# Kernel tuning notes

Measured on AMD Instinct MI355X. Metric: run time of the kernel, lower is better.

## Reference

```python
import jax, jax.numpy as jnp
import numpy as np


def _icosa_group():
    """60 rotation matrices of the icosahedral rotation group (vertex anchors)."""
    phi = (1.0 + 5.0 ** 0.5) / 2.0

    def rot(axis, ang):
        a = np.asarray(axis, dtype=np.float64)
        a = a / np.linalg.norm(a)
        K = np.array([[0.0, -a[2], a[1]], [a[2], 0.0, -a[0]], [-a[1], a[0], 0.0]])
        return np.eye(3) + np.sin(ang) * K + (1.0 - np.cos(ang)) * (K @ K)

    # two distinct 5-fold vertex axes generate the full group of order 60
    gens = [rot([0.0, 1.0, phi], 2.0 * np.pi / 5.0),
            rot([0.0, -1.0, phi], 2.0 * np.pi / 5.0)]
    mats = {tuple(np.round(np.eye(3), 6).ravel()): np.eye(3)}
    frontier = [np.eye(3)]
    while frontier:
        new = []
        for m in frontier:
            for g in gens:
                p = g @ m
                k = tuple(np.round(p, 6).ravel())
                if k not in mats:
                    mats[k] = p
                    new.append(p)
        frontier = new
    Rs = np.stack([mats[k] for k in sorted(mats.keys())]).astype(np.float32)
    assert Rs.shape[0] == 60
    return Rs


def _normalize(x, axis=-1, eps=1e-12):
    n = jnp.linalg.norm(x, axis=axis, keepdims=True)
    return x / jnp.maximum(n, eps)


def setup_inputs() -> dict:
    key = jax.random.key(0)
    ks = jax.random.split(key, 6)
    bs, P, N = 2, 1024, 16
    d_in, d_out, K = 64, 32, 7
    neighbor_index = jax.random.randint(ks[0], (bs, P, N), 0, P, dtype=jnp.int32)
    vertices = jax.random.normal(ks[1], (bs, P, 3), dtype=jnp.float32)
    feature_map = jax.random.normal(ks[2], (bs, d_in, P, 3), dtype=jnp.float32)
    W = jax.random.normal(ks[3], (d_out, d_in, K, 3), dtype=jnp.float32) * (2.0 / (d_in * K * 3 + d_out * K * 3)) ** 0.5
    W_center = jax.random.normal(ks[4], (d_out, d_in), dtype=jnp.float32) * (2.0 / (d_in + d_out)) ** 0.5
    directions = jax.random.normal(ks[5], (d_out, K, 3), dtype=jnp.float32) * (2.0 / (d_out * 3 + K * 3)) ** 0.5
    Rs = jnp.asarray(_icosa_group())
    return {"neighbor_index": neighbor_index, "vertices": vertices,
            "feature_map": feature_map, "W": W, "W_center": W_center,
            "directions": directions, "Rs": Rs}


def reference(neighbor_index, vertices, feature_map, W, W_center, directions, Rs):
    bs, P, N = neighbor_index.shape
    d_out, d_in, K, _ = W.shape
    n_bin = 5
    interval = Rs.shape[0] // n_bin

    # neighbor direction unit vectors [b,p,n,3]
    nbrs = jax.vmap(lambda v_b, i_b: v_b[i_b])(vertices, neighbor_index)
    ndn = _normalize(nbrs - vertices[:, :, None, :])
    kd = _normalize(directions)  # [d,k,3]

    # ---- stage 1: rotation search (fully detached in the torch original) ----
    ndn_s = jax.lax.stop_gradient(ndn)
    kd_s = jax.lax.stop_gradient(kd)
    W_s = jax.lax.stop_gradient(W)
    fm_s = jax.lax.stop_gradient(feature_map)
    Rs_s = jax.lax.stop_gradient(Rs)

    r_vals, r_idxs = [], []
    for i in range(n_bin):
        Rsi = Rs_s[i * interval:(i + 1) * interval]  # [r,3,3]
        kd_ro = jnp.einsum('dkj,rij->dkir', kd_s, Rsi)          # [d,k,3,r]
        theta = jnp.einsum('dkjr,bpnj->bdkpnr', kd_ro, ndn_s)   # [b,d,k,p,n,r]
        W_ro = jnp.einsum('dckj,rij->dckir', W_s, Rsi)          # [d,c,k,3,r]
        fo = jnp.einsum('dckir,bcpi->bdkpr', W_ro, fm_s)        # [b,d,k,p,r]
        gathered = jax.vmap(lambda f_b, i_b: f_b[:, :, i_b, :])(fo, neighbor_index)  # [b,d,k,p,n,r]
        ka = gathered * theta
        ka = jnp.max(ka, axis=4)   # max over neighbors -> [b,d,k,p,r]
        ka = jnp.sum(ka, axis=2)   # sum over kernel pts -> [b,d,p,r]
        r_vals.append(jnp.max(ka, axis=-1))
        r_idxs.append(jnp.argmax(ka, axis=-1) + i * interval)
    r_vals = jnp.stack(r_vals, axis=-1)  # [b,d,p,5]
    r_idxs = jnp.stack(r_idxs, axis=-1)  # [b,d,p,5]
    best_bin = jnp.argmax(r_vals, axis=-1)  # [b,d,p]
    r_index = jnp.take_along_axis(r_idxs, best_bin[..., None], axis=-1)[..., 0]  # [b,d,p]
    match_R = Rs[r_index]  # [b,d,p,3,3]

    # ---- stage 2: apply best rotation (differentiable) ----
    kd_ro2 = jnp.einsum('dkj,bdpij->bdkpi', kd, match_R)               # [b,d,k,p,3]
    theta2 = jax.nn.relu(jnp.einsum('bdkpj,bpnj->bdkpn', kd_ro2, ndn))  # [b,d,k,p,n]
    fo2 = jnp.einsum('dckj,bdpij,bcpi->bdkp', W, match_R, feature_map)  # [b,d,k,p]
    gathered2 = jax.vmap(lambda f_b, i_b: f_b[:, :, i_b])(fo2, neighbor_index)  # [b,d,k,p,n]
    ka2 = gathered2 * theta2
    kaw2 = jnp.max(ka2, axis=4)  # [b,d,k,p]
    out = jnp.einsum('bdkp,bdkpi->bdpi', kaw2, kd_ro2)
    center = jnp.einsum('dc,bcpi->bdpi', W_center, feature_map)
    return out + center
```

## Files before the change

### kernel.cpp

```cpp
#include <hip/hip_runtime.h>
#include <math.h>

#define BS   2
#define PP   1024
#define NN   16
#define CIN  64
#define DOUT 32
#define KK   7
#define NR   60
#define NT2  30

#define OFF_NDN  0
#define OFF_KROT 98304
#define OFF_M    138624
#define OFF_PVAL 4332928
#define OFF_PIDX 6299008
#define OFF_FO2  6790528
#define OFF_RIDX 7314816
#define OFF_CEN  7380352

#define NEG_INF (-3.402823466e38f)

typedef float v2f __attribute__((ext_vector_type(2)));
typedef float v4f __attribute__((ext_vector_type(4)));

__device__ __forceinline__ float sload(const float* __restrict__ p, int idx) {
    return __int_as_float(__builtin_amdgcn_readfirstlane(__float_as_int(p[idx])));
}

__device__ __forceinline__ v2f pk_mul_sv(v2f s, v2f v) {
    v2f d; asm("v_pk_mul_f32 %0, %1, %2" : "=v"(d) : "s"(s), "v"(v)); return d;
}
__device__ __forceinline__ v2f pk_fma_svv(v2f s, v2f v, v2f c) {
    v2f d; asm("v_pk_fma_f32 %0, %1, %2, %3" : "=v"(d) : "s"(s), "v"(v), "v"(c)); return d;
}
__device__ __forceinline__ v2f pk_mul_vv(v2f a, v2f b) {
    v2f d; asm("v_pk_mul_f32 %0, %1, %2" : "=v"(d) : "v"(a), "v"(b)); return d;
}

__device__ __forceinline__ float quad_max(float x) {
    float y = __int_as_float(__builtin_amdgcn_mov_dpp(
        __float_as_int(x), 0xB1, 0xF, 0xF, true));
    x = fmaxf(x, y);
    float z = __int_as_float(__builtin_amdgcn_mov_dpp(
        __float_as_int(x), 0x4E, 0xF, 0xF, true));
    return fmaxf(x, z);
}

__global__ __launch_bounds__(256) void k_pre(const int* __restrict__ nbr,
                                             const float* __restrict__ vert,
                                             const float* __restrict__ dirs,
                                             const float* __restrict__ Rs,
                                             float* __restrict__ ws) {
    int tid = blockIdx.x * 256 + threadIdx.x;
    if (tid < BS * PP * NN) {
        int p = (tid >> 4) & (PP - 1);
        int b = tid >> 14;
        int q = nbr[tid];
        const float* vp = vert + ((b << 10) + p) * 3;
        const float* vq = vert + ((b << 10) + q) * 3;
        float dx = vq[0] - vp[0], dy = vq[1] - vp[1], dz = vq[2] - vp[2];
        float nrm = sqrtf(dx * dx + dy * dy + dz * dz);
        float den = fmaxf(nrm, 1e-12f);
        dx /= den; dy /= den; dz /= den;
        float* o = ws + OFF_NDN + tid * 3;
        o[0] = dx; o[1] = dy; o[2] = dz;
    }
    int t2 = tid - BS * PP * NN;
    if (t2 >= 0 && t2 < DOUT * NR * KK) {
        int k = t2 % KK;
        int r = (t2 / KK) % NR;
        int d = t2 / (KK * NR);
        const float* dk = dirs + (d * KK + k) * 3;
        float x = dk[0], y = dk[1], z = dk[2];
        float nrm = sqrtf(x * x + y * y + z * z);
        float den = fmaxf(nrm, 1e-12f);
        x /= den; y /= den; z /= den;
        const float* R = Rs + r * 9;
        float* o = ws + OFF_KROT + t2 * 3;
        o[0] = R[0] * x + R[1] * y + R[2] * z;
        o[1] = R[3] * x + R[4] * y + R[5] * z;
        o[2] = R[6] * x + R[7] * y + R[8] * z;
    }
}

__global__ __launch_bounds__(256, 2) void k_buildM(const float* __restrict__ fm,
                                                   const float* __restrict__ W,
                                                   const float* __restrict__ Wc,
                                                   float* __restrict__ Mout,
                                                   float* __restrict__ cen) {
    int d = blockIdx.y, b = blockIdx.z;
    int p = blockIdx.x * 256 + threadIdx.x;

    float M[64];
#pragma unroll
    for (int t = 0; t < 64; t++) M[t] = 0.f;
    float c0 = 0.f, c1 = 0.f, c2 = 0.f;

    const float* fbase = fm + (size_t)(b * CIN * PP + p) * 3;
    const float* wbase = W + (size_t)d * CIN * KK * 3;
    const float* wrow = Wc + d * CIN;
    for (int c = 0; c < CIN; c++) {
        const float* f = fbase + c * PP * 3;
        float f0 = f[0], f1 = f[1], f2 = f[2];
        const float* wl = wbase + c * 21;
#pragma unroll
        for (int k = 0; k < KK; k++) {
#pragma unroll
            for (int j = 0; j < 3; j++) {
                float w = sload(wl, k * 3 + j);
                M[k * 9 + 0 + j] += w * f0;
                M[k * 9 + 3 + j] += w * f1;
                M[k * 9 + 6 + j] += w * f2;
            }
        }
        float wcv = sload(wrow, c);
        c0 += wcv * f0; c1 += wcv * f1; c2 += wcv * f2;
    }
    int gid = ((b * DOUT + d) << 10) + p;
    float4* o = (float4*)(Mout + (size_t)gid * 64);
#pragma unroll
    for (int t = 0; t < 15; t++)
        o[t] = make_float4(M[4 * t], M[4 * t + 1], M[4 * t + 2], M[4 * t + 3]);
    o[15] = make_float4(M[60], M[61], M[62], 0.f);
    float* cp = cen + (size_t)gid * 3;
    cp[0] = c0; cp[1] = c1; cp[2] = c2;
}

__device__ __forceinline__ int fo_base(int p) {
    return (p << 2) ^ ((p >> 1) & 7);
}

__global__ __launch_bounds__(1024)
void k_score(const int* __restrict__ nbr,
             const float* __restrict__ Rs,
             const float* __restrict__ Mptr,
             const float* __restrict__ ndn,
             const float* __restrict__ krot,
             float* __restrict__ pval,
             unsigned char* __restrict__ pidx8) {
    __shared__ v4f fo4s[PP * 4];
    const int tile = blockIdx.x, d = blockIdx.y, b = blockIdx.z;
    const int bd = b * DOUT + d;
    const int rbase = tile * 2;
    const int tq = threadIdx.x >> 2;
    const int ns = threadIdx.x & 3;

    {
        const int p = threadIdx.x;
        float Rc0[9], Rc1[9];
#pragma unroll
        for (int j = 0; j < 9; j++) {
            Rc0[j] = sload(Rs, (rbase + 0) * 9 + j);
            Rc1[j] = sload(Rs, (rbase + 1) * 9 + j);
        }
        float fo0[KK], fo1[KK];
#pragma unroll
        for (int k = 0; k < KK; k++) { fo0[k] = 0.f; fo1[k] = 0.f; }

        const float4* m4 = (const float4*)(Mptr + (size_t)((bd << 10) + p) * 64);
#pragma unroll
        for (int t = 0; t < 16; t++) {
            float4 v = m4[t];
            float e[4] = {v.x, v.y, v.z, v.w};
#pragma unroll
            for (int ee = 0; ee < 4; ee++) {
                const int g = 4 * t + ee;
                if (g < 63) {
                    const int k = g / 9, r9 = g % 9;
                    fo0[k] += Rc0[r9] * e[ee];
                    fo1[k] += Rc1[r9] * e[ee];
                }
            }
            if ((t & 3) == 3)
                __builtin_amdgcn_sched_barrier(0);
        }
        const int fb = fo_base(p);
        v4f s0; s0.x = fo0[0]; s0.y = fo1[0]; s0.z = fo0[1]; s0.w = fo1[1];
        v4f s1; s1.x = fo0[2]; s1.y = fo1[2]; s1.z = fo0[3]; s1.w = fo1[3];
        v4f s2; s2.x = fo0[4]; s2.y = fo1[4]; s2.z = fo0[5]; s2.w = fo1[5];
        v4f s3; s3.x = fo0[6]; s3.y = fo1[6]; s3.z = 0.f;    s3.w = 0.f;
        fo4s[fb]     = s0;
        fo4s[fb ^ 1] = s1;
        fo4s[fb ^ 2] = s2;
        fo4s[fb ^ 3] = s3;
    }
    __syncthreads();

    v2f vkp[KK][3];
    {
        const int kb0 = (d * NR + rbase + 0) * 21;
        const int kb1 = (d * NR + rbase + 1) * 21;
#pragma unroll
        for (int k = 0; k < KK; k++)
#pragma unroll
            for (int c = 0; c < 3; c++) {
                v2f t; t.x = sload(krot, kb0 + k * 3 + c);
                       t.y = sload(krot, kb1 + k * 3 + c);
                vkp[k][c] = t;
            }
    }
    const v2f* fo2s = (const v2f*)fo4s;

#pragma unroll
    for (int pp = 0; pp < 4; pp++) {
        const int p2 = (pp << 8) + tq;

        int4 nv = *(const int4*)(nbr + (((size_t)((b << 10) + p2)) << 4) + (ns << 2));
        float u[12];
        {
            const float4* u4 = (const float4*)(ndn + ((size_t)((b << 10) + p2) * 16 + (ns << 2)) * 3);
            float4 a = u4[0], bb = u4[1], cc = u4[2];
            u[0] = a.x;  u[1] = a.y;  u[2] = a.z;  u[3] = a.w;
            u[4] = bb.x; u[5] = bb.y; u[6] = bb.z; u[7] = bb.w;
            u[8] = cc.x; u[9] = cc.y; u[10] = cc.z; u[11] = cc.w;
        }

        float mk0[KK], mk1[KK];
#pragma unroll
        for (int k = 0; k < KK; k++) { mk0[k] = NEG_INF; mk1[k] = NEG_INF; }

        int c0 = fo_base(nv.x);
        v4f A = fo4s[c0];
        v4f B = fo4s[c0 ^ 1];
        v4f C = fo4s[c0 ^ 2];
        v2f D = fo2s[(c0 ^ 3) << 1];

#pragma unroll
        for (int n = 0; n < 4; n++) {
            v4f An, Bn, Cn; v2f Dn;
            if (n < 3) {
                int qn = (n == 0) ? nv.y : (n == 1) ? nv.z : nv.w;
                int cn = fo_base(qn);
                An = fo4s[cn];
                Bn = fo4s[cn ^ 1];
                Cn = fo4s[cn ^ 2];
                Dn = fo2s[(cn ^ 3) << 1];
            }
            float u0 = u[n * 3], u1 = u[n * 3 + 1], u2 = u[n * 3 + 2];
            v2f u00; u00.x = u0; u00.y = u0;
            v2f u11; u11.x = u1; u11.y = u1;
            v2f u22; u22.x = u2; u22.y = u2;
#pragma unroll
            for (int k = 0; k < KK; k++) {
                v2f g;
                if (k == 0)      g = __builtin_shufflevector(A, A, 0, 1);
                else if (k == 1) g = __builtin_shufflevector(A, A, 2, 3);
                else if (k == 2) g = __builtin_shufflevector(B, B, 0, 1);
                else if (k == 3) g = __builtin_shufflevector(B, B, 2, 3);
                else if (k == 4) g = __builtin_shufflevector(C, C, 0, 1);
                else if (k == 5) g = __builtin_shufflevector(C, C, 2, 3);
                else             g = D;
                v2f t = pk_mul_sv(vkp[k][0], u00);
                t = pk_fma_svv(vkp[k][1], u11, t);
                t = pk_fma_svv(vkp[k][2], u22, t);
                v2f pr = pk_mul_vv(g, t);
                mk0[k] = fmaxf(mk0[k], pr.x);
                mk1[k] = fmaxf(mk1[k], pr.y);
            }
            if (n < 3) { A = An; B = Bn; C = Cn; D = Dn; }
            __builtin_amdgcn_sched_barrier(0);
        }
#pragma unroll
        for (int k = 0; k < KK; k++) {
            mk0[k] = quad_max(mk0[k]);
            mk1[k] = quad_max(mk1[k]);
        }
        float s0 = ((mk0[0] + mk0[1]) + (mk0[2] + mk0[3])) + ((mk0[4] + mk0[5]) + mk0[6]);
        float s1 = ((mk1[0] + mk1[1]) + (mk1[2] + mk1[3])) + ((mk1[4] + mk1[5]) + mk1[6]);
        float bl = s0; int bil = rbase;
        if (s1 > bl) { bl = s1; bil = rbase + 1; }

        if (ns == 0) {
            int pi = (bd * NT2 + tile) * PP + p2;
            pval[pi] = bl;
            pidx8[pi] = (unsigned char)bil;
        }
    }
}

__global__ __launch_bounds__(256, 2) void k_reduce(const float* __restrict__ Rs,
                                                   float* __restrict__ ws) {
    int gid = blockIdx.x * 256 + threadIdx.x;
    int bd = gid >> 10;
    int p = gid & (PP - 1);
    const unsigned char* pidx8 = (const unsigned char*)(ws + OFF_PIDX);
    float best = NEG_INF;
    int bi = 0;
    for (int t = 0; t < NT2; t++) {
        float v = ws[OFF_PVAL + (bd * NT2 + t) * PP + p];
        int idx = pidx8[(bd * NT2 + t) * PP + p];
        if (v > best) { best = v; bi = idx; }
    }
    ((int*)ws)[OFF_RIDX + gid] = bi;

    const float* R = Rs + bi * 9;
    float R0 = R[0], R1 = R[1], R2 = R[2];
    float R3 = R[3], R4 = R[4], R5 = R[5];
    float R6 = R[6], R7 = R[7], R8 = R[8];

    float M[64];
    const float4* m4 = (const float4*)(ws + OFF_M + (size_t)gid * 64);
#pragma unroll
    for (int t = 0; t < 16; t++) {
        float4 v = m4[t];
        M[4 * t] = v.x; M[4 * t + 1] = v.y; M[4 * t + 2] = v.z; M[4 * t + 3] = v.w;
    }
    float* o = ws + OFF_FO2 + (size_t)gid * 8;
#pragma unroll
    for (int k = 0; k < KK; k++) {
        o[k] = R0 * M[k * 9 + 0] + R1 * M[k * 9 + 1] + R2 * M[k * 9 + 2]
             + R3 * M[k * 9 + 3] + R4 * M[k * 9 + 4] + R5 * M[k * 9 + 5]
             + R6 * M[k * 9 + 6] + R7 * M[k * 9 + 7] + R8 * M[k * 9 + 8];
    }
    o[7] = 0.f;
}

__global__ __launch_bounds__(256, 2) void k_final(const int* __restrict__ nbr,
                                                  const float* __restrict__ ws,
                                                  float* __restrict__ out) {
    __shared__ float fo2_s[PP * 8];
    __shared__ float krot_s[NR * KK * 3];
    int d = blockIdx.y, b = blockIdx.z;
    int bd = b * DOUT + d;
    for (int i = threadIdx.x; i < PP * 8; i += 256)
        fo2_s[i] = ws[OFF_FO2 + (size_t)bd * PP * 8 + i];
    for (int i = threadIdx.x; i < NR * KK * 3; i += 256)
        krot_s[i] = ws[OFF_KROT + d * NR * KK * 3 + i];
    __syncthreads();

    int p = blockIdx.x * 256 + threadIdx.x;
    int gid = (bd << 10) + p;
    int ri = ((const int*)ws)[OFF_RIDX + gid];

    float v[21];
#pragma unroll
    for (int t = 0; t < 21; t++) v[t] = krot_s[ri * 21 + t];

    float u[48];
    {
        const float4* u4 = (const float4*)(ws + OFF_NDN + (size_t)((b << 10) + p) * 48);
#pragma unroll
        for (int t = 0; t < 12; t++) {
            float4 w = u4[t];
            u[4 * t] = w.x; u[4 * t + 1] = w.y; u[4 * t + 2] = w.z; u[4 * t + 3] = w.w;
        }
    }
    int nidx[16];
    {
        const int4* n4 = (const int4*)(nbr + (size_t)((b << 10) + p) * 16);
#pragma unroll
        for (int t = 0; t < 4; t++) {
            int4 w = n4[t];
            nidx[4 * t] = w.x; nidx[4 * t + 1] = w.y; nidx[4 * t + 2] = w.z; nidx[4 * t + 3] = w.w;
        }
    }

    float kaw[7];
#pragma unroll
    for (int k = 0; k < KK; k++) kaw[k] = NEG_INF;
#pragma unroll
    for (int n = 0; n < NN; n++) {
        int q = nidx[n];
        const float4* fq = (const float4*)&fo2_s[q * 8];
        float4 a = fq[0], c4 = fq[1];
        float g[7] = {a.x, a.y, a.z, a.w, c4.x, c4.y, c4.z};
        float u0 = u[n * 3], u1 = u[n * 3 + 1], u2 = u[n * 3 + 2];
#pragma unroll
        for (int k = 0; k < KK; k++) {
            float th = fmaxf(v[k * 3] * u0 + v[k * 3 + 1] * u1 + v[k * 3 + 2] * u2, 0.f);
            kaw[k] = fmaxf(kaw[k], g[k] * th);
        }
    }
    float o0 = 0.f, o1 = 0.f, o2 = 0.f;
#pragma unroll
    for (int k = 0; k < KK; k++) {
        o0 += kaw[k] * v[k * 3];
        o1 += kaw[k] * v[k * 3 + 1];
        o2 += kaw[k] * v[k * 3 + 2];
    }
    const float* cp = ws + OFF_CEN + (size_t)gid * 3;
    out[(size_t)gid * 3 + 0] = o0 + cp[0];
    out[(size_t)gid * 3 + 1] = o1 + cp[1];
    out[(size_t)gid * 3 + 2] = o2 + cp[2];
}

extern "C" void kernel_launch(void* const* d_in, const int* in_sizes, int n_in,
                              void* d_out, int out_size, void* d_ws, size_t ws_size,
                              hipStream_t stream) {
    const int*   nbr  = (const int*)d_in[0];
    const float* vert = (const float*)d_in[1];
    const float* fm   = (const float*)d_in[2];
    const float* W    = (const float*)d_in[3];
    const float* Wc   = (const float*)d_in[4];
    const float* dirs = (const float*)d_in[5];
    const float* Rs   = (const float*)d_in[6];
    float* ws  = (float*)d_ws;
    float* out = (float*)d_out;

    k_pre<<<181, 256, 0, stream>>>(nbr, vert, dirs, Rs, ws);
    k_buildM<<<dim3(PP / 256, DOUT, BS), 256, 0, stream>>>(
        fm, W, Wc, ws + OFF_M, ws + OFF_CEN);
    k_score<<<dim3(NT2, DOUT, BS), 1024, 0, stream>>>(
        nbr, Rs, ws + OFF_M, ws + OFF_NDN, ws + OFF_KROT,
        ws + OFF_PVAL, (unsigned char*)(ws + OFF_PIDX));
    k_reduce<<<dim3(BS * DOUT * PP / 256), 256, 0, stream>>>(Rs, ws);
    k_final<<<dim3(PP / 256, DOUT, BS), 256, 0, stream>>>(nbr, ws, out);
}
```

Measured before the change: 161.5 us.

## Merge preprocessing and M-build kernels; deepen LDS gather prefetch to two neighbors

Folds k_pre and k_buildM into one k_prebuild launch, with a block-ID split: the first 256 blocks build M and the center term, the rest compute normalized neighbor directions and rotated kernel directions. This removes one kernel launch and lets the two independent workloads run at the same time. In k_score, the neighbor feature gather from LDS now prefetches two neighbors ahead instead of one, to hide LDS latency. The deeper prefetch costs extra registers in a 1024-thread block.

New measurement: 182.0 us. 12.7% more time.

```diff
diff --git a/kernel.cpp b/kernel.cpp
--- a/kernel.cpp
+++ b/kernel.cpp
@@ -47,84 +47,85 @@
     return fmaxf(x, z);
 }
 
-__global__ __launch_bounds__(256) void k_pre(const int* __restrict__ nbr,
-                                             const float* __restrict__ vert,
-                                             const float* __restrict__ dirs,
-                                             const float* __restrict__ Rs,
-                                             float* __restrict__ ws) {
-    int tid = blockIdx.x * 256 + threadIdx.x;
-    if (tid < BS * PP * NN) {
-        int p = (tid >> 4) & (PP - 1);
-        int b = tid >> 14;
-        int q = nbr[tid];
-        const float* vp = vert + ((b << 10) + p) * 3;
-        const float* vq = vert + ((b << 10) + q) * 3;
-        float dx = vq[0] - vp[0], dy = vq[1] - vp[1], dz = vq[2] - vp[2];
-        float nrm = sqrtf(dx * dx + dy * dy + dz * dz);
-        float den = fmaxf(nrm, 1e-12f);
-        dx /= den; dy /= den; dz /= den;
-        float* o = ws + OFF_NDN + tid * 3;
-        o[0] = dx; o[1] = dy; o[2] = dz;
-    }
-    int t2 = tid - BS * PP * NN;
-    if (t2 >= 0 && t2 < DOUT * NR * KK) {
-        int k = t2 % KK;
-        int r = (t2 / KK) % NR;
-        int d = t2 / (KK * NR);
-        const float* dk = dirs + (d * KK + k) * 3;
-        float x = dk[0], y = dk[1], z = dk[2];
-        float nrm = sqrtf(x * x + y * y + z * z);
-        float den = fmaxf(nrm, 1e-12f);
-        x /= den; y /= den; z /= den;
-        const float* R = Rs + r * 9;
-        float* o = ws + OFF_KROT + t2 * 3;
-        o[0] = R[0] * x + R[1] * y + R[2] * z;
-        o[1] = R[3] * x + R[4] * y + R[5] * z;
-        o[2] = R[6] * x + R[7] * y + R[8] * z;
-    }
-}
-
-__global__ __launch_bounds__(256, 2) void k_buildM(const float* __restrict__ fm,
-                                                   const float* __restrict__ W,
-                                                   const float* __restrict__ Wc,
-                                                   float* __restrict__ Mout,
-                                                   float* __restrict__ cen) {
-    int d = blockIdx.y, b = blockIdx.z;
-    int p = blockIdx.x * 256 + threadIdx.x;
-
-    float M[64];
-#pragma unroll
-    for (int t = 0; t < 64; t++) M[t] = 0.f;
-    float c0 = 0.f, c1 = 0.f, c2 = 0.f;
-
-    const float* fbase = fm + (size_t)(b * CIN * PP + p) * 3;
-    const float* wbase = W + (size_t)d * CIN * KK * 3;
-    const float* wrow = Wc + d * CIN;
-    for (int c = 0; c < CIN; c++) {
-        const float* f = fbase + c * PP * 3;
-        float f0 = f[0], f1 = f[1], f2 = f[2];
-        const float* wl = wbase + c * 21;
-#pragma unroll
-        for (int k = 0; k < KK; k++) {
-#pragma unroll
-            for (int j = 0; j < 3; j++) {
-                float w = sload(wl, k * 3 + j);
-                M[k * 9 + 0 + j] += w * f0;
-                M[k * 9 + 3 + j] += w * f1;
-                M[k * 9 + 6 + j] += w * f2;
+__global__ __launch_bounds__(256, 2) void k_prebuild(
+        const int* __restrict__ nbr,
+        const float* __restrict__ vert,
+        const float* __restrict__ dirs,
+        const float* __restrict__ Rs,
+        const float* __restrict__ fm,
+        const float* __restrict__ W,
+        const float* __restrict__ Wc,
+        float* __restrict__ ws) {
+    int id = blockIdx.x;
+    if (id < 256) {
+        int px = id & 3, d = (id >> 2) & 31, b = id >> 7;
+        int p = px * 256 + threadIdx.x;
+
+        float M[64];
+#pragma unroll
+        for (int t = 0; t < 64; t++) M[t] = 0.f;
+        float c0 = 0.f, c1 = 0.f, c2 = 0.f;
+
+        const float* fbase = fm + (size_t)(b * CIN * PP + p) * 3;
+        const float* wbase = W + (size_t)d * CIN * KK * 3;
+        const float* wrow = Wc + d * CIN;
+        for (int c = 0; c < CIN; c++) {
+            const float* f = fbase + c * PP * 3;
+            float f0 = f[0], f1 = f[1], f2 = f[2];
+            const float* wl = wbase + c * 21;
+#pragma unroll
+            for (int k = 0; k < KK; k++) {
+#pragma unroll
+                for (int j = 0; j < 3; j++) {
+                    float w = sload(wl, k * 3 + j);
+                    M[k * 9 + 0 + j] += w * f0;
+                    M[k * 9 + 3 + j] += w * f1;
+                    M[k * 9 + 6 + j] += w * f2;
+                }
             }
-        }
-        float wcv = sload(wrow, c);
-        c0 += wcv * f0; c1 += wcv * f1; c2 += wcv * f2;
-    }
-    int gid = ((b * DOUT + d) << 10) + p;
-    float4* o = (float4*)(Mout + (size_t)gid * 64);
-#pragma unroll
-    for (int t = 0; t < 15; t++)
-        o[t] = make_float4(M[4 * t], M[4 * t + 1], M[4 * t + 2], M[4 * t + 3]);
-    o[15] = make_float4(M[60], M[61], M[62], 0.f);
-    float* cp = cen + (size_t)gid * 3;
-    cp[0] = c0; cp[1] = c1; cp[2] = c2;
+            float wcv = sload(wrow, c);
+            c0 += wcv * f0; c1 += wcv * f1; c2 += wcv * f2;
+        }
+        int gid = ((b * DOUT + d) << 10) + p;
+        float4* o = (float4*)(ws + OFF_M + (size_t)gid * 64);
+#pragma unroll
+        for (int t = 0; t < 15; t++)
+            o[t] = make_float4(M[4 * t], M[4 * t + 1], M[4 * t + 2], M[4 * t + 3]);
+        o[15] = make_float4(M[60], M[61], M[62], 0.f);
+        float* cp = ws + OFF_CEN + (size_t)gid * 3;
+        cp[0] = c0; cp[1] = c1; cp[2] = c2;
+    } else {
+        int tid = (id - 256) * 256 + threadIdx.x;
+        if (tid < BS * PP * NN) {
+            int p = (tid >> 4) & (PP - 1);
+            int b = tid >> 14;
+            int q = nbr[tid];
+            const float* vp = vert + ((b << 10) + p) * 3;
+            const float* vq = vert + ((b << 10) + q) * 3;
+            float dx = vq[0] - vp[0], dy = vq[1] - vp[1], dz = vq[2] - vp[2];
+            float nrm = sqrtf(dx * dx + dy * dy + dz * dz);
+            float den = fmaxf(nrm, 1e-12f);
+            dx /= den; dy /= den; dz /= den;
+            float* o = ws + OFF_NDN + tid * 3;
+            o[0] = dx; o[1] = dy; o[2] = dz;
+        }
+        int t2 = tid - BS * PP * NN;
+        if (t2 >= 0 && t2 < DOUT * NR * KK) {
+            int k = t2 % KK;
+            int r = (t2 / KK) % NR;
+            int d = t2 / (KK * NR);
+            const float* dk = dirs + (d * KK + k) * 3;
+            float x = dk[0], y = dk[1], z = dk[2];
+            float nrm = sqrtf(x * x + y * y + z * z);
+            float den = fmaxf(nrm, 1e-12f);
+            x /= den; y /= den; z /= den;
+            const float* R = Rs + r * 9;
+            float* o = ws + OFF_KROT + t2 * 3;
+            o[0] = R[0] * x + R[1] * y + R[2] * z;
+            o[1] = R[3] * x + R[4] * y + R[5] * z;
+            o[2] = R[6] * x + R[7] * y + R[8] * z;
+        }
+    }
 }
 
 __device__ __forceinline__ int fo_base(int p) {
@@ -220,22 +221,25 @@
 #pragma unroll
         for (int k = 0; k < KK; k++) { mk0[k] = NEG_INF; mk1[k] = NEG_INF; }
 
-        int c0 = fo_base(nv.x);
-        v4f A = fo4s[c0];
-        v4f B = fo4s[c0 ^ 1];
-        v4f C = fo4s[c0 ^ 2];
-        v2f D = fo2s[(c0 ^ 3) << 1];
+        v4f Aa, Ba, Ca; v2f Da;
+        v4f Ab, Bb, Cb; v2f Db;
+        {
+            int c0 = fo_base(nv.x);
+            Aa = fo4s[c0]; Ba = fo4s[c0 ^ 1]; Ca = fo4s[c0 ^ 2];
+            Da = fo2s[(c0 ^ 3) << 1];
+            int c1 = fo_base(nv.y);
+            Ab = fo4s[c1]; Bb = fo4s[c1 ^ 1]; Cb = fo4s[c1 ^ 2];
+            Db = fo2s[(c1 ^ 3) << 1];
+        }
 
 #pragma unroll
         for (int n = 0; n < 4; n++) {
-            v4f An, Bn, Cn; v2f Dn;
-            if (n < 3) {
-                int qn = (n == 0) ? nv.y : (n == 1) ? nv.z : nv.w;
+            v4f Ac, Bc, Cc; v2f Dc;
+            if (n < 2) {
+                int qn = (n == 0) ? nv.z : nv.w;
                 int cn = fo_base(qn);
-                An = fo4s[cn];
-                Bn = fo4s[cn ^ 1];
-                Cn = fo4s[cn ^ 2];
-                Dn = fo2s[(cn ^ 3) << 1];
+                Ac = fo4s[cn]; Bc = fo4s[cn ^ 1]; Cc = fo4s[cn ^ 2];
+                Dc = fo2s[(cn ^ 3) << 1];
             }
             float u0 = u[n * 3], u1 = u[n * 3 + 1], u2 = u[n * 3 + 2];
             v2f u00; u00.x = u0; u00.y = u0;
@@ -244,13 +248,13 @@
 #pragma unroll
             for (int k = 0; k < KK; k++) {
                 v2f g;
-                if (k == 0)      g = __builtin_shufflevector(A, A, 0, 1);
-                else if (k == 1) g = __builtin_shufflevector(A, A, 2, 3);
-                else if (k == 2) g = __builtin_shufflevector(B, B, 0, 1);
-                else if (k == 3) g = __builtin_shufflevector(B, B, 2, 3);
-                else if (k == 4) g = __builtin_shufflevector(C, C, 0, 1);
-                else if (k == 5) g = __builtin_shufflevector(C, C, 2, 3);
-                else             g = D;
+                if (k == 0)      g = __builtin_shufflevector(Aa, Aa, 0, 1);
+                else if (k == 1) g = __builtin_shufflevector(Aa, Aa, 2, 3);
+                else if (k == 2) g = __builtin_shufflevector(Ba, Ba, 0, 1);
+                else if (k == 3) g = __builtin_shufflevector(Ba, Ba, 2, 3);
+                else if (k == 4) g = __builtin_shufflevector(Ca, Ca, 0, 1);
+                else if (k == 5) g = __builtin_shufflevector(Ca, Ca, 2, 3);
+                else             g = Da;
                 v2f t = pk_mul_sv(vkp[k][0], u00);
                 t = pk_fma_svv(vkp[k][1], u11, t);
                 t = pk_fma_svv(vkp[k][2], u22, t);
@@ -258,7 +262,8 @@
                 mk0[k] = fmaxf(mk0[k], pr.x);
                 mk1[k] = fmaxf(mk1[k], pr.y);
             }
-            if (n < 3) { A = An; B = Bn; C = Cn; D = Dn; }
+            Aa = Ab; Ba = Bb; Ca = Cb; Da = Db;
+            if (n < 2) { Ab = Ac; Bb = Bc; Cb = Cc; Db = Dc; }
             __builtin_amdgcn_sched_barrier(0);
         }
 #pragma unroll
@@ -398,9 +403,7 @@
     float* ws  = (float*)d_ws;
     float* out = (float*)d_out;
 
-    k_pre<<<181, 256, 0, stream>>>(nbr, vert, dirs, Rs, ws);
-    k_buildM<<<dim3(PP / 256, DOUT, BS), 256, 0, stream>>>(
-        fm, W, Wc, ws + OFF_M, ws + OFF_CEN);
+    k_prebuild<<<437, 256, 0, stream>>>(nbr, vert, dirs, Rs, fm, W, Wc, ws);
     k_score<<<dim3(NT2, DOUT, BS), 1024, 0, stream>>>(
         nbr, Rs, ws + OFF_M, ws + OFF_NDN, ws + OFF_KROT,
         ws + OFF_PVAL, (unsigned char*)(ws + OFF_PIDX));
```
